# Optimization experiments

Hardware: AMD Instinct MI355X
Metric: run time of the kernel (lower is better)

The kernel has to match this reference:

```python
import jax, jax.numpy as jnp
import numpy as np

D_MODEL, D_FF, N_EXPERTS, TOP_K = 1024, 4096, 8, 2

def setup_inputs() -> dict:
    key = jax.random.key(0)
    k1, k2, k3, k4 = jax.random.split(key, 4)
    x = jax.random.normal(k1, (4, 2048, D_MODEL), dtype=jnp.float32)
    # glorot-ish scaled init for weights
    router = jax.random.normal(k2, (D_MODEL, N_EXPERTS), dtype=jnp.float32) * (1.0 / np.sqrt(D_MODEL))
    W1 = jax.random.normal(k3, (N_EXPERTS, D_MODEL, D_FF), dtype=jnp.float32) * (1.0 / np.sqrt(D_MODEL))
    W2 = jax.random.normal(k4, (N_EXPERTS, D_FF, D_MODEL), dtype=jnp.float32) * (1.0 / np.sqrt(D_FF))
    return {"x": x, "router": router, "W1": W1, "W2": W2}

def reference(x, router, W1, W2):
    B, S, d = x.shape
    E = router.shape[1]
    xf = x.reshape(-1, d)                              # [T, d]
    logits = xf @ router                               # [T, E]
    top_v, top_i = jax.lax.top_k(logits, TOP_K)        # [T, k]
    w = jax.nn.softmax(top_v, axis=-1)                 # softmax over selected experts
    # scatter top-k weights into a dense [T, E] gate matrix (indices are distinct)
    gates = jnp.sum(jax.nn.one_hot(top_i, E, dtype=x.dtype) * w[..., None], axis=1)
    out = jnp.zeros_like(xf)
    for e in range(E):                                 # small fixed expert loop
        h = xf @ W1[e]                                 # [T, d_ff]
        h = h * jax.nn.sigmoid(h)                      # swish
        out = out + gates[:, e:e + 1] * (h @ W2[e])    # weighted combine
    return out.reshape(B, S, d)
```

## Files before the change

kernel.cpp:

```cpp
#include <hip/hip_runtime.h>
#include <hip/hip_bf16.h>

#define NTOK 8192
#define DM 1024
#define DFF 4096
#define NE 8

typedef __attribute__((ext_vector_type(8))) short bf16x8;
typedef __attribute__((ext_vector_type(4))) float f32x4;

__device__ __forceinline__ ushort f2bf(float f) {
  __hip_bfloat16 h = __float2bfloat16(f);
  return *reinterpret_cast<ushort*>(&h);
}

__global__ void cvt_x_kernel(const float* __restrict__ x, ushort* __restrict__ xb) {
  int i = blockIdx.x * 256 + threadIdx.x;
  float4 v = reinterpret_cast<const float4*>(x)[i];
  ushort4 o;
  o.x = f2bf(v.x); o.y = f2bf(v.y); o.z = f2bf(v.z); o.w = f2bf(v.w);
  reinterpret_cast<ushort4*>(xb)[i] = o;
}

__global__ void transpose_cvt(const float* __restrict__ in, ushort* __restrict__ out,
                              int R, int C) {
  __shared__ float t[64][65];
  const float* inp = in + (size_t)blockIdx.z * R * C;
  ushort* op = out + (size_t)blockIdx.z * R * C;
  int c0 = blockIdx.x * 64, r0 = blockIdx.y * 64;
  int tid = threadIdx.x;
#pragma unroll
  for (int it = 0; it < 4; ++it) {
    int r = it * 16 + (tid >> 4);
    int c = (tid & 15) * 4;
    float4 v = *reinterpret_cast<const float4*>(inp + (size_t)(r0 + r) * C + c0 + c);
    t[r][c] = v.x; t[r][c + 1] = v.y; t[r][c + 2] = v.z; t[r][c + 3] = v.w;
  }
  __syncthreads();
  int c = tid >> 2, rc = (tid & 3) * 16;
  union { ushort us[16]; uint4 q[2]; } u;
#pragma unroll
  for (int i = 0; i < 16; ++i) u.us[i] = f2bf(t[rc + i][c]);
  uint4* dst = reinterpret_cast<uint4*>(op + (size_t)(c0 + c) * R + r0 + rc);
  dst[0] = u.q[0];
  dst[1] = u.q[1];
}

__global__ void router_kernel(const float* __restrict__ x, const float* __restrict__ router,
                              int* __restrict__ cnt, int* __restrict__ list,
                              float* __restrict__ wa) {
  __shared__ float rl[DM * NE];
  int tid = threadIdx.x;
  for (int i = tid; i < DM * NE / 4; i += 256)
    reinterpret_cast<float4*>(rl)[i] = reinterpret_cast<const float4*>(router)[i];
  __syncthreads();
  int wave = tid >> 6, lane = tid & 63;
  int tok0 = blockIdx.x * 32 + wave * 8;
  for (int tI = 0; tI < 8; ++tI) {
    int tok = tok0 + tI;
    float acc[NE];
#pragma unroll
    for (int e2 = 0; e2 < NE; ++e2) acc[e2] = 0.f;
    const float4* xr = reinterpret_cast<const float4*>(x + (size_t)tok * DM);
#pragma unroll
    for (int c = 0; c < 4; ++c) {
      float4 v = xr[lane * 4 + c];
      int d = lane * 16 + c * 4;
      const float* vv = reinterpret_cast<const float*>(&v);
#pragma unroll
      for (int q = 0; q < 4; ++q) {
        float xv = vv[q];
#pragma unroll
        for (int e2 = 0; e2 < NE; ++e2) acc[e2] += xv * rl[(d + q) * NE + e2];
      }
    }
    for (int off = 32; off > 0; off >>= 1) {
#pragma unroll
      for (int e2 = 0; e2 < NE; ++e2) acc[e2] += __shfl_xor(acc[e2], off, 64);
    }
    if (lane == 0) {
      int i0 = 0; float v0 = acc[0];
#pragma unroll
      for (int e2 = 1; e2 < NE; ++e2) { if (acc[e2] > v0) { v0 = acc[e2]; i0 = e2; } }
      int i1 = -1; float v1 = -3.4e38f;
#pragma unroll
      for (int e2 = 0; e2 < NE; ++e2) { if (e2 != i0 && acc[e2] > v1) { v1 = acc[e2]; i1 = e2; } }
      float e1 = expf(v1 - v0);
      float w0 = 1.f / (1.f + e1);
      float w1 = e1 / (1.f + e1);
      int s0 = atomicAdd(&cnt[i0], 1);
      list[i0 * NTOK + s0] = tok * 2;
      wa[tok * 2] = w0;
      int s1 = atomicAdd(&cnt[i1], 1);
      list[i1 * NTOK + s1] = tok * 2 + 1;
      wa[tok * 2 + 1] = w1;
    }
  }
}

__device__ __forceinline__ void gl_lds16(const void* g, void* s) {
  __builtin_amdgcn_global_load_lds(
      (const __attribute__((address_space(1))) unsigned int*)g,
      (__attribute__((address_space(3))) unsigned int*)s, 16, 0, 0);
}

template <int PASS>
__launch_bounds__(256, 2)
__global__ void moe_gemm(const ushort* __restrict__ Abase,
                         const ushort* __restrict__ Wt,
                         const int* __restrict__ cnt,
                         const int* __restrict__ list,
                         const float* __restrict__ wa,
                         ushort* __restrict__ H,
                         float* __restrict__ out) {
  constexpr int K = (PASS == 1) ? DM : DFF;
  constexpr int NB = (PASS == 1) ? DFF : DM;
  const int e = blockIdx.z;
  const int n = cnt[e];
  const int tTile = blockIdx.y;
  if (tTile * 128 >= n) return;
  const int nTile = blockIdx.x;

  __shared__ __attribute__((aligned(16))) char As[128 * 128];
  __shared__ __attribute__((aligned(16))) char Bs[128 * 128];
  __shared__ int aL[128];
  __shared__ unsigned long long pL[128];

  const int tid = threadIdx.x;
  if (tid < 128) {
    int slot = tTile * 128 + tid;
    int sl = (slot < n) ? slot : (n - 1);
    int a = list[e * NTOK + sl];
    aL[tid] = (slot < n) ? a : -1;
    size_t row = (PASS == 1) ? (size_t)(a >> 1) : (size_t)a;
    pL[tid] = (unsigned long long)(Abase + row * K);
  }
  __syncthreads();

  const int wv = tid >> 6, lane = tid & 63;
  unsigned long long srcA[4], srcB[4];
  unsigned int dstOff[4];
  const char* WtE = (const char*)(Wt + (size_t)e * NB * K);
#pragma unroll
  for (int i = 0; i < 4; ++i) {
    int row = wv * 32 + i * 8 + (lane >> 3);
    int cb = ((lane & 7) * 16) ^ ((row & 7) << 4);
    srcA[i] = pL[row] + cb;
    srcB[i] = (unsigned long long)(WtE + ((size_t)(nTile * 128 + row) * K) * 2 + cb);
    dstOff[i] = row * 128 + (lane & 7) * 16;
  }

  f32x4 acc[4][4];
#pragma unroll
  for (int m = 0; m < 4; ++m)
#pragma unroll
    for (int nn = 0; nn < 4; ++nn) acc[m][nn] = (f32x4){0.f, 0.f, 0.f, 0.f};

  const int r0 = (wv >> 1) * 64, c0 = (wv & 1) * 64;

  for (int kt = 0; kt < K / 64; ++kt) {
#pragma unroll
    for (int i = 0; i < 4; ++i) {
      gl_lds16((const void*)srcA[i], As + dstOff[i]);
      gl_lds16((const void*)srcB[i], Bs + dstOff[i]);
      srcA[i] += 128;
      srcB[i] += 128;
    }
    __syncthreads();
#pragma unroll
    for (int kk = 0; kk < 2; ++kk) {
      bf16x8 af[4], bf[4];
#pragma unroll
      for (int m = 0; m < 4; ++m) {
        int row = r0 + m * 16 + (lane & 15);
        int kb = (kk * 32 + (lane >> 4) * 8) * 2;
        af[m] = *reinterpret_cast<const bf16x8*>(As + row * 128 + (kb ^ ((row & 7) << 4)));
      }
#pragma unroll
      for (int nn = 0; nn < 4; ++nn) {
        int row = c0 + nn * 16 + (lane & 15);
        int kb = (kk * 32 + (lane >> 4) * 8) * 2;
        bf[nn] = *reinterpret_cast<const bf16x8*>(Bs + row * 128 + (kb ^ ((row & 7) << 4)));
      }
#pragma unroll
      for (int m = 0; m < 4; ++m)
#pragma unroll
        for (int nn = 0; nn < 4; ++nn)
          acc[m][nn] = __builtin_amdgcn_mfma_f32_16x16x32_bf16(af[m], bf[nn], acc[m][nn], 0, 0, 0);
    }
    __syncthreads();
  }

#pragma unroll
  for (int m = 0; m < 4; ++m) {
#pragma unroll
    for (int j = 0; j < 4; ++j) {
      int lr = r0 + m * 16 + (lane >> 4) * 4 + j;
      int a = aL[lr];
      if (a < 0) continue;
      if (PASS == 1) {
        ushort* hrow = H + (size_t)a * DFF + nTile * 128 + c0 + (lane & 15);
#pragma unroll
        for (int nn = 0; nn < 4; ++nn) {
          float v = acc[m][nn][j];
          float sw = v / (1.f + expf(-v));
          hrow[nn * 16] = f2bf(sw);
        }
      } else {
        float w = wa[a];
        int tok = a >> 1;
        float* orow = out + (size_t)tok * DM + nTile * 128 + c0 + (lane & 15);
#pragma unroll
        for (int nn = 0; nn < 4; ++nn)
          atomicAdd(&orow[nn * 16], w * acc[m][nn][j]);
      }
    }
  }
}

extern "C" void kernel_launch(void* const* d_in, const int* in_sizes, int n_in,
                              void* d_out, int out_size, void* d_ws, size_t ws_size,
                              hipStream_t stream) {
  const float* x = (const float*)d_in[0];
  const float* router = (const float*)d_in[1];
  const float* W1 = (const float*)d_in[2];
  const float* W2 = (const float*)d_in[3];
  float* out = (float*)d_out;
  char* ws = (char*)d_ws;

  size_t off = 0;
  ushort* Xb = (ushort*)(ws + off); off += (size_t)NTOK * DM * 2;
  ushort* Wt1 = (ushort*)(ws + off); off += (size_t)NE * DM * DFF * 2;
  ushort* Wt2 = (ushort*)(ws + off); off += (size_t)NE * DM * DFF * 2;
  ushort* H   = (ushort*)(ws + off); off += (size_t)NTOK * 2 * DFF * 2;
  int* cnt  = (int*)(ws + off); off += 256;
  int* list = (int*)(ws + off); off += (size_t)NE * NTOK * 4;
  float* wa = (float*)(ws + off); off += (size_t)NTOK * 2 * 4;

  hipMemsetAsync(out, 0, (size_t)NTOK * DM * sizeof(float), stream);
  hipMemsetAsync(cnt, 0, NE * sizeof(int), stream);

  cvt_x_kernel<<<NTOK * DM / 4 / 256, 256, 0, stream>>>(x, Xb);
  transpose_cvt<<<dim3(DFF / 64, DM / 64, NE), 256, 0, stream>>>(W1, Wt1, DM, DFF);
  transpose_cvt<<<dim3(DM / 64, DFF / 64, NE), 256, 0, stream>>>(W2, Wt2, DFF, DM);
  router_kernel<<<NTOK / 32, 256, 0, stream>>>(x, router, cnt, list, wa);

  moe_gemm<1><<<dim3(DFF / 128, NTOK / 128, NE), 256, 0, stream>>>(Xb, Wt1, cnt, list, wa, H, out);
  moe_gemm<2><<<dim3(DM / 128, NTOK / 128, NE), 256, 0, stream>>>(H, Wt2, cnt, list, wa, H, out);
}
```

Baseline: 698.0 us.

## Pipeline MoE GEMM with 4-stage async LDS ring and larger 512-thread tiles

Rewrites the grouped expert GEMM main loop to use a four-slot LDS ring filled by direct global-to-LDS loads, so three K-slices are in flight while MFMAs consume the current one. Completion is tracked with explicit vmcnt waits and raw barriers. Tiles grow to 256 columns with 512 threads, and M is 256 for pass 1 and 128 for pass 2, which raises data reuse per block. The swizzle is removed and the K-slice per stage shrinks to 32, which risks LDS bank conflicts, and the larger LDS footprint may lower occupancy.

Result: slower. 872.2 us (+25.0%).

```diff
diff --git a/kernel.cpp b/kernel.cpp
--- a/kernel.cpp
+++ b/kernel.cpp
@@ -98,37 +98,50 @@
   }
 }
 
-__device__ __forceinline__ void gl_lds16(const void* g, void* s) {
+__device__ __forceinline__ void gl_lds16(unsigned long long g, void* s) {
   __builtin_amdgcn_global_load_lds(
       (const __attribute__((address_space(1))) unsigned int*)g,
       (__attribute__((address_space(3))) unsigned int*)s, 16, 0, 0);
 }
 
-template <int PASS>
-__launch_bounds__(256, 2)
+#define WAITV(N) asm volatile("s_waitcnt vmcnt(" #N ")" ::: "memory")
+
+__device__ __forceinline__ void BARRIER() {
+  asm volatile("" ::: "memory");
+  __builtin_amdgcn_s_barrier();
+  asm volatile("" ::: "memory");
+}
+
+template <int PASS, int MFR>
+__launch_bounds__(512, 2)
 __global__ void moe_gemm(const ushort* __restrict__ Abase,
                          const ushort* __restrict__ Wt,
                          const int* __restrict__ cnt,
                          const int* __restrict__ list,
                          const float* __restrict__ wa,
-                         ushort* __restrict__ H,
+                         ushort* __restrict__ Hbuf,
                          float* __restrict__ out) {
   constexpr int K = (PASS == 1) ? DM : DFF;
   constexpr int NB = (PASS == 1) ? DFF : DM;
+  constexpr int BM = MFR * 32;
+  constexpr int NPH = K / 32;
+  constexpr int AL = BM / 128;
+  constexpr int ASLOT = BM * 64;
+
   const int e = blockIdx.z;
   const int n = cnt[e];
   const int tTile = blockIdx.y;
-  if (tTile * 128 >= n) return;
+  if (tTile * BM >= n) return;
   const int nTile = blockIdx.x;
 
-  __shared__ __attribute__((aligned(16))) char As[128 * 128];
-  __shared__ __attribute__((aligned(16))) char Bs[128 * 128];
-  __shared__ int aL[128];
-  __shared__ unsigned long long pL[128];
+  __shared__ __attribute__((aligned(16))) char As[4 * ASLOT];
+  __shared__ __attribute__((aligned(16))) char Bs[4 * 16384];
+  __shared__ int aL[BM];
+  __shared__ unsigned long long pL[BM];
 
   const int tid = threadIdx.x;
-  if (tid < 128) {
-    int slot = tTile * 128 + tid;
+  if (tid < BM) {
+    int slot = tTile * BM + tid;
     int sl = (slot < n) ? slot : (n - 1);
     int a = list[e * NTOK + sl];
     aL[tid] = (slot < n) ? a : -1;
@@ -137,79 +150,100 @@
   }
   __syncthreads();
 
+  const char* WtE = (const char*)(Wt + (size_t)e * NB * K);
+  const int r4 = tid >> 2;
+  const int colb = (tid & 3) * 16;
+  unsigned long long sA[AL];
+  unsigned long long sB[2];
+#pragma unroll
+  for (int j = 0; j < AL; ++j) sA[j] = pL[j * 128 + r4] + colb;
+#pragma unroll
+  for (int j = 0; j < 2; ++j)
+    sB[j] = (unsigned long long)WtE + (size_t)(nTile * 256 + j * 128 + r4) * K * 2 + colb;
+  const unsigned dOff = tid * 16;
+
+  auto STAGE = [&](int s) {
+#pragma unroll
+    for (int j = 0; j < AL; ++j) {
+      gl_lds16(sA[j], As + s * ASLOT + j * 8192 + dOff);
+      sA[j] += 64;
+    }
+#pragma unroll
+    for (int j = 0; j < 2; ++j) {
+      gl_lds16(sB[j], Bs + s * 16384 + j * 8192 + dOff);
+      sB[j] += 64;
+    }
+  };
+
   const int wv = tid >> 6, lane = tid & 63;
-  unsigned long long srcA[4], srcB[4];
-  unsigned int dstOff[4];
-  const char* WtE = (const char*)(Wt + (size_t)e * NB * K);
-#pragma unroll
-  for (int i = 0; i < 4; ++i) {
-    int row = wv * 32 + i * 8 + (lane >> 3);
-    int cb = ((lane & 7) * 16) ^ ((row & 7) << 4);
-    srcA[i] = pL[row] + cb;
-    srcB[i] = (unsigned long long)(WtE + ((size_t)(nTile * 128 + row) * K) * 2 + cb);
-    dstOff[i] = row * 128 + (lane & 7) * 16;
-  }
-
-  f32x4 acc[4][4];
-#pragma unroll
-  for (int m = 0; m < 4; ++m)
+  const int wm = wv >> 2, wn = wv & 3;
+  const unsigned aBase = (unsigned)(wm * MFR * 16 + (lane & 15)) * 64 + (lane >> 4) * 16;
+  const unsigned bBase = (unsigned)(wn * 64 + (lane & 15)) * 64 + (lane >> 4) * 16;
+
+  f32x4 acc[MFR][4];
+#pragma unroll
+  for (int m = 0; m < MFR; ++m)
 #pragma unroll
     for (int nn = 0; nn < 4; ++nn) acc[m][nn] = (f32x4){0.f, 0.f, 0.f, 0.f};
 
-  const int r0 = (wv >> 1) * 64, c0 = (wv & 1) * 64;
-
-  for (int kt = 0; kt < K / 64; ++kt) {
-#pragma unroll
-    for (int i = 0; i < 4; ++i) {
-      gl_lds16((const void*)srcA[i], As + dstOff[i]);
-      gl_lds16((const void*)srcB[i], Bs + dstOff[i]);
-      srcA[i] += 128;
-      srcB[i] += 128;
-    }
-    __syncthreads();
-#pragma unroll
-    for (int kk = 0; kk < 2; ++kk) {
-      bf16x8 af[4], bf[4];
-#pragma unroll
-      for (int m = 0; m < 4; ++m) {
-        int row = r0 + m * 16 + (lane & 15);
-        int kb = (kk * 32 + (lane >> 4) * 8) * 2;
-        af[m] = *reinterpret_cast<const bf16x8*>(As + row * 128 + (kb ^ ((row & 7) << 4)));
-      }
-#pragma unroll
-      for (int nn = 0; nn < 4; ++nn) {
-        int row = c0 + nn * 16 + (lane & 15);
-        int kb = (kk * 32 + (lane >> 4) * 8) * 2;
-        bf[nn] = *reinterpret_cast<const bf16x8*>(Bs + row * 128 + (kb ^ ((row & 7) << 4)));
-      }
-#pragma unroll
-      for (int m = 0; m < 4; ++m)
-#pragma unroll
-        for (int nn = 0; nn < 4; ++nn)
-          acc[m][nn] = __builtin_amdgcn_mfma_f32_16x16x32_bf16(af[m], bf[nn], acc[m][nn], 0, 0, 0);
-    }
-    __syncthreads();
-  }
-
-#pragma unroll
-  for (int m = 0; m < 4; ++m) {
+  auto PHASE = [&](int s) {
+    const char* a_ = As + s * ASLOT;
+    const char* b_ = Bs + s * 16384;
+    bf16x8 af[MFR], bfr[4];
+#pragma unroll
+    for (int m = 0; m < MFR; ++m)
+      af[m] = *reinterpret_cast<const bf16x8*>(a_ + aBase + m * 16 * 64);
+#pragma unroll
+    for (int nn = 0; nn < 4; ++nn)
+      bfr[nn] = *reinterpret_cast<const bf16x8*>(b_ + bBase + nn * 16 * 64);
+    __builtin_amdgcn_s_setprio(1);
+#pragma unroll
+    for (int m = 0; m < MFR; ++m)
+#pragma unroll
+      for (int nn = 0; nn < 4; ++nn)
+        acc[m][nn] = __builtin_amdgcn_mfma_f32_16x16x32_bf16(af[m], bfr[nn], acc[m][nn], 0, 0, 0);
+    __builtin_amdgcn_s_setprio(0);
+    asm volatile("s_waitcnt lgkmcnt(0)" ::: "memory");
+    __builtin_amdgcn_s_barrier();
+    asm volatile("" ::: "memory");
+  };
+
+  STAGE(0); STAGE(1); STAGE(2);
+#pragma unroll 4
+  for (int h = 0; h < NPH - 3; ++h) {
+    STAGE((h + 3) & 3);
+    if constexpr (MFR == 8) { WAITV(12); } else { WAITV(9); }
+    BARRIER();
+    PHASE(h & 3);
+  }
+  if constexpr (MFR == 8) { WAITV(8); } else { WAITV(6); }
+  BARRIER();
+  PHASE((NPH - 3) & 3);
+  if constexpr (MFR == 8) { WAITV(4); } else { WAITV(3); }
+  BARRIER();
+  PHASE((NPH - 2) & 3);
+  WAITV(0);
+  BARRIER();
+  PHASE((NPH - 1) & 3);
+
+#pragma unroll
+  for (int m = 0; m < MFR; ++m) {
 #pragma unroll
     for (int j = 0; j < 4; ++j) {
-      int lr = r0 + m * 16 + (lane >> 4) * 4 + j;
+      int lr = wm * MFR * 16 + m * 16 + (lane >> 4) * 4 + j;
       int a = aL[lr];
       if (a < 0) continue;
       if (PASS == 1) {
-        ushort* hrow = H + (size_t)a * DFF + nTile * 128 + c0 + (lane & 15);
+        ushort* hrow = Hbuf + (size_t)a * DFF + nTile * 256 + wn * 64 + (lane & 15);
 #pragma unroll
         for (int nn = 0; nn < 4; ++nn) {
           float v = acc[m][nn][j];
-          float sw = v / (1.f + expf(-v));
-          hrow[nn * 16] = f2bf(sw);
+          hrow[nn * 16] = f2bf(v / (1.f + expf(-v)));
         }
       } else {
         float w = wa[a];
         int tok = a >> 1;
-        float* orow = out + (size_t)tok * DM + nTile * 128 + c0 + (lane & 15);
+        float* orow = out + (size_t)tok * DM + nTile * 256 + wn * 64 + (lane & 15);
 #pragma unroll
         for (int nn = 0; nn < 4; ++nn)
           atomicAdd(&orow[nn * 16], w * acc[m][nn][j]);
@@ -245,6 +279,6 @@
   transpose_cvt<<<dim3(DM / 64, DFF / 64, NE), 256, 0, stream>>>(W2, Wt2, DFF, DM);
   router_kernel<<<NTOK / 32, 256, 0, stream>>>(x, router, cnt, list, wa);
 
-  moe_gemm<1><<<dim3(DFF / 128, NTOK / 128, NE), 256, 0, stream>>>(Xb, Wt1, cnt, list, wa, H, out);
-  moe_gemm<2><<<dim3(DM / 128, NTOK / 128, NE), 256, 0, stream>>>(H, Wt2, cnt, list, wa, H, out);
-}
+  moe_gemm<1, 8><<<dim3(DFF / 256, NTOK / 256, NE), 512, 0, stream>>>(Xb, Wt1, cnt, list, wa, H, out);
+  moe_gemm<2, 4><<<dim3(DM / 256, NTOK / 128, NE), 512, 0, stream>>>(H, Wt2, cnt, list, wa, H, out);
+}
```

## Pipeline MoE GEMM with triple-buffered LDS, 128x256 tiles and compact tile table

Applied to the files above, without the earlier changes.

Replaces the single-buffered GEMM loop with a three-stage global-to-LDS pipeline using explicit vmcnt waits, so loads for upcoming K-steps overlap the MFMA work. Tiles grow to 128x256 with 512 threads (8 waves), and the MFMA section is wrapped in s_setprio. A new build_tiles kernel compacts the active (expert, token-tile) pairs into a table, so the grid no longer launches mostly-empty blocks across all experts. The larger LDS footprint (about 144KB) may limit occupancy to a single block per CU, and the extra launch adds a little overhead.

Result: slower. 947.3 us (+35.7%).

```diff
diff --git a/kernel.cpp b/kernel.cpp
--- a/kernel.cpp
+++ b/kernel.cpp
@@ -5,6 +5,7 @@
 #define DM 1024
 #define DFF 4096
 #define NE 8
+#define MAXT 136
 
 typedef __attribute__((ext_vector_type(8))) short bf16x8;
 typedef __attribute__((ext_vector_type(4))) float f32x4;
@@ -98,31 +99,47 @@
   }
 }
 
-__device__ __forceinline__ void gl_lds16(const void* g, void* s) {
+__global__ void build_tiles(const int* __restrict__ cnt, unsigned* __restrict__ table) {
+  if (threadIdx.x == 0) {
+    int t = 0;
+    for (int e = 0; e < NE; ++e) {
+      int nt = (cnt[e] + 127) >> 7;
+      for (int i = 0; i < nt; ++i) table[t++] = ((unsigned)e << 16) | (unsigned)i;
+    }
+    for (; t < MAXT; ++t) table[t] = 0xFFFFFFFFu;
+  }
+}
+
+__device__ __forceinline__ void gl_lds16(unsigned long long g, void* s) {
   __builtin_amdgcn_global_load_lds(
       (const __attribute__((address_space(1))) unsigned int*)g,
       (__attribute__((address_space(3))) unsigned int*)s, 16, 0, 0);
 }
 
 template <int PASS>
-__launch_bounds__(256, 2)
+__launch_bounds__(512, 2)
 __global__ void moe_gemm(const ushort* __restrict__ Abase,
                          const ushort* __restrict__ Wt,
                          const int* __restrict__ cnt,
                          const int* __restrict__ list,
+                         const unsigned* __restrict__ table,
                          const float* __restrict__ wa,
-                         ushort* __restrict__ H,
+                         ushort* __restrict__ Hbuf,
                          float* __restrict__ out) {
   constexpr int K = (PASS == 1) ? DM : DFF;
-  constexpr int NB = (PASS == 1) ? DFF : DM;
-  const int e = blockIdx.z;
+  constexpr int NK = K / 64;
+  constexpr int ASLOT = 128 * 128;
+  constexpr int BSLOT = 256 * 128;
+
+  unsigned td = table[blockIdx.y];
+  if (td == 0xFFFFFFFFu) return;
+  const int e = td >> 16;
+  const int tTile = td & 0xFFFF;
   const int n = cnt[e];
-  const int tTile = blockIdx.y;
-  if (tTile * 128 >= n) return;
   const int nTile = blockIdx.x;
 
-  __shared__ __attribute__((aligned(16))) char As[128 * 128];
-  __shared__ __attribute__((aligned(16))) char Bs[128 * 128];
+  __shared__ __attribute__((aligned(16))) char As[3 * ASLOT];
+  __shared__ __attribute__((aligned(16))) char Bs[3 * BSLOT];
   __shared__ int aL[128];
   __shared__ unsigned long long pL[128];
 
@@ -137,18 +154,34 @@
   }
   __syncthreads();
 
+  const char* WtE = (const char*)(Wt + (size_t)e * ((size_t)(PASS == 1 ? DFF : DM)) * K);
+  const int sr = tid >> 3;
+  const int sc = (tid & 7) * 16;
+  unsigned long long sA[2], sB[4];
+  unsigned dA[2], dB[4];
+#pragma unroll
+  for (int j = 0; j < 2; ++j) {
+    int row = j * 64 + sr;
+    sA[j] = pL[row] + (unsigned)(sc ^ ((row & 7) << 4));
+    dA[j] = (unsigned)(row * 128 + sc);
+  }
+#pragma unroll
+  for (int j = 0; j < 4; ++j) {
+    int row = j * 64 + sr;
+    sB[j] = (unsigned long long)WtE + (size_t)(nTile * 256 + row) * (K * 2) +
+            (unsigned)(sc ^ ((row & 7) << 4));
+    dB[j] = (unsigned)(row * 128 + sc);
+  }
+
+  auto STAGE = [&](int s) {
+#pragma unroll
+    for (int j = 0; j < 2; ++j) { gl_lds16(sA[j], As + s * ASLOT + dA[j]); sA[j] += 128; }
+#pragma unroll
+    for (int j = 0; j < 4; ++j) { gl_lds16(sB[j], Bs + s * BSLOT + dB[j]); sB[j] += 128; }
+  };
+
   const int wv = tid >> 6, lane = tid & 63;
-  unsigned long long srcA[4], srcB[4];
-  unsigned int dstOff[4];
-  const char* WtE = (const char*)(Wt + (size_t)e * NB * K);
-#pragma unroll
-  for (int i = 0; i < 4; ++i) {
-    int row = wv * 32 + i * 8 + (lane >> 3);
-    int cb = ((lane & 7) * 16) ^ ((row & 7) << 4);
-    srcA[i] = pL[row] + cb;
-    srcB[i] = (unsigned long long)(WtE + ((size_t)(nTile * 128 + row) * K) * 2 + cb);
-    dstOff[i] = row * 128 + (lane & 7) * 16;
-  }
+  const int wm = wv >> 2, wn = wv & 3;
 
   f32x4 acc[4][4];
 #pragma unroll
@@ -156,60 +189,73 @@
 #pragma unroll
     for (int nn = 0; nn < 4; ++nn) acc[m][nn] = (f32x4){0.f, 0.f, 0.f, 0.f};
 
-  const int r0 = (wv >> 1) * 64, c0 = (wv & 1) * 64;
-
-  for (int kt = 0; kt < K / 64; ++kt) {
-#pragma unroll
-    for (int i = 0; i < 4; ++i) {
-      gl_lds16((const void*)srcA[i], As + dstOff[i]);
-      gl_lds16((const void*)srcB[i], Bs + dstOff[i]);
-      srcA[i] += 128;
-      srcB[i] += 128;
-    }
-    __syncthreads();
+  auto COMPUTE = [&](int s) {
+    const char* a_ = As + s * ASLOT;
+    const char* b_ = Bs + s * BSLOT;
 #pragma unroll
     for (int kk = 0; kk < 2; ++kk) {
-      bf16x8 af[4], bf[4];
+      const int kb = kk * 64 + (lane >> 4) * 16;
+      bf16x8 af[4], bfr[4];
 #pragma unroll
       for (int m = 0; m < 4; ++m) {
-        int row = r0 + m * 16 + (lane & 15);
-        int kb = (kk * 32 + (lane >> 4) * 8) * 2;
-        af[m] = *reinterpret_cast<const bf16x8*>(As + row * 128 + (kb ^ ((row & 7) << 4)));
+        int row = wm * 64 + m * 16 + (lane & 15);
+        af[m] = *reinterpret_cast<const bf16x8*>(a_ + row * 128 + (kb ^ ((row & 7) << 4)));
       }
 #pragma unroll
       for (int nn = 0; nn < 4; ++nn) {
-        int row = c0 + nn * 16 + (lane & 15);
-        int kb = (kk * 32 + (lane >> 4) * 8) * 2;
-        bf[nn] = *reinterpret_cast<const bf16x8*>(Bs + row * 128 + (kb ^ ((row & 7) << 4)));
-      }
+        int row = wn * 64 + nn * 16 + (lane & 15);
+        bfr[nn] = *reinterpret_cast<const bf16x8*>(b_ + row * 128 + (kb ^ ((row & 7) << 4)));
+      }
+      __builtin_amdgcn_s_setprio(1);
 #pragma unroll
       for (int m = 0; m < 4; ++m)
 #pragma unroll
         for (int nn = 0; nn < 4; ++nn)
-          acc[m][nn] = __builtin_amdgcn_mfma_f32_16x16x32_bf16(af[m], bf[nn], acc[m][nn], 0, 0, 0);
-    }
-    __syncthreads();
+          acc[m][nn] = __builtin_amdgcn_mfma_f32_16x16x32_bf16(af[m], bfr[nn], acc[m][nn], 0, 0, 0);
+      __builtin_amdgcn_s_setprio(0);
+    }
+  };
+
+  STAGE(0);
+  STAGE(1);
+  int c = 0;
+  for (int kt = 0; kt < NK; ++kt) {
+    if (kt + 2 < NK) {
+      int ss = c + 2; if (ss >= 3) ss -= 3;
+      STAGE(ss);
+      asm volatile("s_waitcnt vmcnt(12)" ::: "memory");
+    } else if (kt + 1 < NK) {
+      asm volatile("s_waitcnt vmcnt(6)" ::: "memory");
+    } else {
+      asm volatile("s_waitcnt vmcnt(0)" ::: "memory");
+    }
+    __builtin_amdgcn_s_barrier();
+    asm volatile("" ::: "memory");
+    COMPUTE(c);
+    asm volatile("" ::: "memory");
+    __builtin_amdgcn_s_barrier();
+    asm volatile("" ::: "memory");
+    c = (c == 2) ? 0 : c + 1;
   }
 
 #pragma unroll
   for (int m = 0; m < 4; ++m) {
 #pragma unroll
     for (int j = 0; j < 4; ++j) {
-      int lr = r0 + m * 16 + (lane >> 4) * 4 + j;
+      int lr = wm * 64 + m * 16 + (lane >> 4) * 4 + j;
       int a = aL[lr];
       if (a < 0) continue;
       if (PASS == 1) {
-        ushort* hrow = H + (size_t)a * DFF + nTile * 128 + c0 + (lane & 15);
+        ushort* hrow = Hbuf + (size_t)a * DFF + nTile * 256 + wn * 64 + (lane & 15);
 #pragma unroll
         for (int nn = 0; nn < 4; ++nn) {
           float v = acc[m][nn][j];
-          float sw = v / (1.f + expf(-v));
-          hrow[nn * 16] = f2bf(sw);
+          hrow[nn * 16] = f2bf(v / (1.f + expf(-v)));
         }
       } else {
         float w = wa[a];
         int tok = a >> 1;
-        float* orow = out + (size_t)tok * DM + nTile * 128 + c0 + (lane & 15);
+        float* orow = out + (size_t)tok * DM + nTile * 256 + wn * 64 + (lane & 15);
 #pragma unroll
         for (int nn = 0; nn < 4; ++nn)
           atomicAdd(&orow[nn * 16], w * acc[m][nn][j]);
@@ -236,6 +282,7 @@
   int* cnt  = (int*)(ws + off); off += 256;
   int* list = (int*)(ws + off); off += (size_t)NE * NTOK * 4;
   float* wa = (float*)(ws + off); off += (size_t)NTOK * 2 * 4;
+  unsigned* table = (unsigned*)(ws + off); off += MAXT * 4;
 
   hipMemsetAsync(out, 0, (size_t)NTOK * DM * sizeof(float), stream);
   hipMemsetAsync(cnt, 0, NE * sizeof(int), stream);
@@ -244,7 +291,8 @@
   transpose_cvt<<<dim3(DFF / 64, DM / 64, NE), 256, 0, stream>>>(W1, Wt1, DM, DFF);
   transpose_cvt<<<dim3(DM / 64, DFF / 64, NE), 256, 0, stream>>>(W2, Wt2, DFF, DM);
   router_kernel<<<NTOK / 32, 256, 0, stream>>>(x, router, cnt, list, wa);
-
-  moe_gemm<1><<<dim3(DFF / 128, NTOK / 128, NE), 256, 0, stream>>>(Xb, Wt1, cnt, list, wa, H, out);
-  moe_gemm<2><<<dim3(DM / 128, NTOK / 128, NE), 256, 0, stream>>>(H, Wt2, cnt, list, wa, H, out);
-}
+  build_tiles<<<1, 64, 0, stream>>>(cnt, table);
+
+  moe_gemm<1><<<dim3(DFF / 256, MAXT), 512, 0, stream>>>(Xb, Wt1, cnt, list, table, wa, H, out);
+  moe_gemm<2><<<dim3(DM / 256, MAXT), 512, 0, stream>>>(H, Wt2, cnt, list, table, wa, H, out);
+}
```
